# Optimization experiments

Hardware: AMD Instinct MI355X
Metric: run time of the kernel (lower is better)

Reference implementation:

```python
import jax, jax.numpy as jnp
import numpy as np

NUM_HEADS = 4
BN_EPS = 1e-5


def setup_inputs() -> dict:
    key = jax.random.key(0)
    k1, k2, k3 = jax.random.split(key, 3)
    B, C, H, W = 4, 512, 64, 64
    c_attn = 256
    x = jax.random.normal(k1, (B, C, H, W), dtype=jnp.float32)
    # 1x1 convs are plain channel matmuls: weight[out, in]
    w_qkv = jax.random.normal(k2, (3 * c_attn, c_attn), dtype=jnp.float32) * (c_attn ** -0.5)
    w_proj = jax.random.normal(k3, (c_attn, c_attn), dtype=jnp.float32) * (c_attn ** -0.5)
    gamma = jnp.ones((c_attn,), dtype=jnp.float32)
    beta = jnp.zeros((c_attn,), dtype=jnp.float32)
    return {"x": x, "w_qkv": w_qkv, "w_proj": w_proj, "gamma": gamma, "beta": beta}


def reference(x, w_qkv, w_proj, gamma, beta):
    B, C, H, W = x.shape
    c_attn = w_proj.shape[0]
    head_dim = c_attn // NUM_HEADS
    scale = head_dim ** -0.5
    N = H * W

    x_attn = x[:, :c_attn].reshape(B, c_attn, N)   # [B, c_attn, N]
    x_skip = x[:, c_attn:]                          # [B, c_skip, H, W]

    # 1x1 conv qkv (no bias): [B, 3*c_attn, N]
    qkv = jnp.einsum('oc,bcn->bon', w_qkv, x_attn)
    qkv = qkv.reshape(B, 3, NUM_HEADS, head_dim, N)
    q, k, v = qkv[:, 0], qkv[:, 1], qkv[:, 2]       # each [B, h, d, N]

    # attn[b,h,i,j] = sum_d q[b,h,d,i] * k[b,h,d,j] * scale
    attn = jnp.einsum('bhdn,bhdm->bhnm', q, k) * scale
    attn = jax.nn.softmax(attn, axis=-1)

    # out[b,h,d,i] = sum_j attn[b,h,i,j] * v[b,h,d,j]
    out = jnp.einsum('bhnm,bhdm->bhdn', attn, v).reshape(B, c_attn, N)

    # 1x1 conv proj (no bias)
    out = jnp.einsum('oc,bcn->bon', w_proj, out)

    # BatchNorm2d (training mode: batch statistics over B and spatial dims)
    mean = out.mean(axis=(0, 2), keepdims=True)
    var = out.var(axis=(0, 2), keepdims=True)  # biased variance, as torch BN
    out = (out - mean) * jax.lax.rsqrt(var + BN_EPS)
    out = out * gamma[None, :, None] + beta[None, :, None]

    out = out.reshape(B, c_attn, H, W)
    return jnp.concatenate([out, x_skip], axis=1)
```

## Files before the change

### kernel.cpp

```cpp
#include <hip/hip_runtime.h>
#include <stdint.h>

typedef float          f32x4  __attribute__((ext_vector_type(4)));
typedef __bf16         bf16x8 __attribute__((ext_vector_type(8)));
typedef unsigned short u16x4  __attribute__((ext_vector_type(4)));
typedef unsigned short u16x8  __attribute__((ext_vector_type(8)));

__device__ __forceinline__ float bf2f(unsigned short u) {
    union { uint32_t i; float f; } v; v.i = ((uint32_t)u) << 16; return v.f;
}
__device__ __forceinline__ unsigned short bfc(float f) {
    return __builtin_bit_cast(unsigned short, (__bf16)f);
}
__device__ __forceinline__ f32x4 mfma16(bf16x8 a, bf16x8 b, f32x4 c) {
    return __builtin_amdgcn_mfma_f32_16x16x32_bf16(a, b, c, 0, 0, 0);
}
__device__ __forceinline__ void async16(const unsigned short* g, unsigned short* l) {
    __builtin_amdgcn_global_load_lds(
        (const __attribute__((address_space(1))) void*)g,
        (__attribute__((address_space(3))) void*)l, 16, 0, 0);
}

#define QSC 0.18033688f

__global__ __launch_bounds__(256) void qkv_gemm(
    const float* __restrict__ x, const float* __restrict__ wqkv,
    unsigned short* __restrict__ Qb, unsigned short* __restrict__ Kb,
    unsigned short* __restrict__ Vb) {
    const int flat = (blockIdx.z * 32 + blockIdx.y) * 6 + blockIdx.x;
    const int v = (flat & 7) * 96 + (flat >> 3);
    const int mt = v % 6;
    const int rest = v / 6;
    const int nt = rest & 31;
    const int b  = rest >> 5;
    const int o0 = mt * 128, n0 = nt * 128;
    __shared__ __align__(16) unsigned short Wt[128 * 72];
    __shared__ __align__(16) unsigned short Xt[128 * 72];
    const int t = threadIdx.x;
    const int lane = t & 63, w = t >> 6;
    const int wr = w >> 1, wc = w & 1;
    const int l15 = lane & 15, g = lane >> 4;

    f32x4 acc[4][4];
    const f32x4 zero = {0.f, 0.f, 0.f, 0.f};
    for (int i = 0; i < 4; i++) for (int j = 0; j < 4; j++) acc[i][j] = zero;

    for (int k0 = 0; k0 < 256; k0 += 64) {
        {
            const int row = t >> 3, col = (t & 7) * 8;
            #pragma unroll
            for (int r = 0; r < 4; r++) {
                const float* p = wqkv + (size_t)(o0 + row + r * 32) * 256 + k0 + col;
                f32x4 v0 = *(const f32x4*)p;
                f32x4 v1 = *(const f32x4*)(p + 4);
                u16x8 o8 = { bfc(v0[0]), bfc(v0[1]), bfc(v0[2]), bfc(v0[3]),
                             bfc(v1[0]), bfc(v1[1]), bfc(v1[2]), bfc(v1[3]) };
                *(u16x8*)(&Wt[(row + r * 32) * 72 + col]) = o8;
            }
        }
        {
            const int cl = t >> 4, nl = (t & 15) * 8;
            const int xw = (t & 7) << 3;
            #pragma unroll
            for (int r = 0; r < 4; r++) {
                const int c = k0 + cl + r * 16;
                const int colw = (cl + r * 16) ^ xw;
                const float* p = x + (size_t)(b * 512 + c) * 4096 + n0 + nl;
                f32x4 v0 = *(const f32x4*)p;
                f32x4 v1 = *(const f32x4*)(p + 4);
                #pragma unroll
                for (int j = 0; j < 4; j++) Xt[(nl + j) * 72 + colw] = bfc(v0[j]);
                #pragma unroll
                for (int j = 0; j < 4; j++) Xt[(nl + 4 + j) * 72 + colw] = bfc(v1[j]);
            }
        }
        __syncthreads();
        #pragma unroll
        for (int kk = 0; kk < 2; kk++) {
            bf16x8 af[4], bfr[4];
            #pragma unroll
            for (int i = 0; i < 4; i++)
                af[i] = *(const bf16x8*)(&Wt[(wr * 64 + i * 16 + l15) * 72 + kk * 32 + g * 8]);
            #pragma unroll
            for (int j = 0; j < 4; j++) {
                const int rrow = wc * 64 + j * 16 + l15;
                const int xr = (((rrow >> 3) & 7) << 3);
                bfr[j] = *(const bf16x8*)(&Xt[rrow * 72 + ((kk * 32 + g * 8) ^ xr)]);
            }
            #pragma unroll
            for (int i = 0; i < 4; i++)
                #pragma unroll
                for (int j = 0; j < 4; j++)
                    acc[i][j] = mfma16(af[i], bfr[j], acc[i][j]);
        }
        __syncthreads();
    }

    #pragma unroll
    for (int i = 0; i < 4; i++) {
        const int o = o0 + wr * 64 + i * 16 + g * 4;
        #pragma unroll
        for (int j = 0; j < 4; j++) {
            const int n = n0 + wc * 64 + j * 16 + l15;
            f32x4 a = acc[i][j];
            if (o < 256) {
                u16x4 pv = { bfc(a[0] * QSC), bfc(a[1] * QSC), bfc(a[2] * QSC), bfc(a[3] * QSC) };
                const int h = o >> 6, d = o & 63;
                *(u16x4*)(&Qb[(((size_t)(b * 4 + h)) * 4096 + n) * 64 + d]) = pv;
            } else if (o < 512) {
                u16x4 pv = { bfc(a[0]), bfc(a[1]), bfc(a[2]), bfc(a[3]) };
                const int oo = o - 256; const int h = oo >> 6, d = oo & 63;
                *(u16x4*)(&Kb[(((size_t)(b * 4 + h)) * 4096 + n) * 64 + d]) = pv;
            } else {
                const int oo = o - 512; const int h = oo >> 6, d = oo & 63;
                const size_t base = (((size_t)(b * 4 + h)) * 64 + d) * 4096 + n;
                Vb[base] = bfc(a[0]); Vb[base + 4096] = bfc(a[1]);
                Vb[base + 8192] = bfc(a[2]); Vb[base + 12288] = bfc(a[3]);
            }
        }
    }
}

__global__ __launch_bounds__(256, 2) void flash_attn(
    const unsigned short* __restrict__ Qb, const unsigned short* __restrict__ Kb,
    const unsigned short* __restrict__ Vb, unsigned short* __restrict__ Opart,
    float* __restrict__ ml) {
    __shared__ __align__(16) unsigned short Kt[2][64 * 64];
    __shared__ __align__(16) unsigned short Vt[2][64 * 64];

    const int flat = (blockIdx.z * 16 + blockIdx.y) * 16 + blockIdx.x;
    const int nf = (flat & 7) * 64 + (flat >> 3);
    const int z  = nf >> 8;
    const int bh = (nf >> 4) & 15;
    const int nb = nf & 15;

    const int t = threadIdx.x, lane = t & 63, w = t >> 6;
    const int l15 = lane & 15, g = lane >> 4;
    const int xo = (l15 & 7) << 3;
    const int c0 = (g * 8) ^ xo, c1 = c0 ^ 32;
    const int vq = ((((g >> 1) ^ (l15 & 7)) << 3) | ((g & 1) << 2));

    const int rb = lane >> 3;
    const int cbe = ((lane & 7) ^ rb) << 3;
    const unsigned short* kgp = Kb + ((size_t)bh * 4096 + z * 2048 + w * 8 + rb) * 64 + cbe;
    const unsigned short* vgp = Vb + ((size_t)(bh * 64 + w * 8 + rb)) * 4096 + z * 2048 + cbe;

    auto stage = [&](int buf) {
        async16(kgp,          &Kt[buf][w * 512]);
        async16(kgp + 2048,   &Kt[buf][w * 512 + 2048]);
        async16(vgp,          &Vt[buf][w * 512]);
        async16(vgp + 131072, &Vt[buf][w * 512 + 2048]);
        kgp += 4096; vgp += 64;
    };

    bf16x8 qf[4][2];
    #pragma unroll
    for (int ntl = 0; ntl < 4; ++ntl) {
        const int nq = nb * 256 + w * 64 + ntl * 16 + l15;
        const unsigned short* qp = Qb + ((size_t)bh * 4096 + nq) * 64;
        qf[ntl][0] = *(const bf16x8*)(qp + g * 8);
        qf[ntl][1] = *(const bf16x8*)(qp + 32 + g * 8);
    }

    const bf16x8 ones8 = __builtin_bit_cast(bf16x8,
        (u16x8){0x3F80, 0x3F80, 0x3F80, 0x3F80, 0x3F80, 0x3F80, 0x3F80, 0x3F80});

    f32x4 of[4][4];
    f32x4 lf[4];
    const f32x4 zero = {0.f, 0.f, 0.f, 0.f};
    #pragma unroll
    for (int dt = 0; dt < 4; ++dt)
        #pragma unroll
        for (int ntl = 0; ntl < 4; ++ntl) of[dt][ntl] = zero;
    lf[0] = zero; lf[1] = zero; lf[2] = zero; lf[3] = zero;

    stage(0);
    __syncthreads();

    for (int itp = 0; itp < 16; ++itp) {
        #pragma unroll
        for (int cur = 0; cur < 2; ++cur) {
            if (itp * 2 + cur < 31) stage(cur ^ 1);

            bf16x8 ka[4][2], va[4][2];
            #pragma unroll
            for (int mt = 0; mt < 4; ++mt) {
                const int kro = (mt * 16 + l15) * 64;
                ka[mt][0] = *(const bf16x8*)(&Kt[cur][kro + c0]);
                ka[mt][1] = *(const bf16x8*)(&Kt[cur][kro + c1]);
            }
            #pragma unroll
            for (int dt = 0; dt < 4; ++dt) {
                const unsigned short* vr = &Vt[cur][l15 * 64 + dt * 1024];
                u16x4 w00 = *(const u16x4*)(vr + (vq ^ 0));
                u16x4 w01 = *(const u16x4*)(vr + (vq ^ 16));
                u16x4 w10 = *(const u16x4*)(vr + (vq ^ 32));
                u16x4 w11 = *(const u16x4*)(vr + (vq ^ 48));
                va[dt][0] = __builtin_bit_cast(bf16x8,
                    __builtin_shufflevector(w00, w01, 0, 1, 2, 3, 4, 5, 6, 7));
                va[dt][1] = __builtin_bit_cast(bf16x8,
                    __builtin_shufflevector(w10, w11, 0, 1, 2, 3, 4, 5, 6, 7));
            }

            #pragma unroll
            for (int ntl = 0; ntl < 4; ++ntl) {
                f32x4 st[4];
                __builtin_amdgcn_s_setprio(1);
                #pragma unroll
                for (int mt = 0; mt < 4; ++mt)
                    st[mt] = mfma16(ka[mt][1], qf[ntl][1],
                                    mfma16(ka[mt][0], qf[ntl][0], zero));
                __builtin_amdgcn_s_setprio(0);

                u16x4 q0 = { bfc(__builtin_amdgcn_exp2f(st[0][0])),
                             bfc(__builtin_amdgcn_exp2f(st[0][1])),
                             bfc(__builtin_amdgcn_exp2f(st[0][2])),
                             bfc(__builtin_amdgcn_exp2f(st[0][3])) };
                u16x4 q1 = { bfc(__builtin_amdgcn_exp2f(st[1][0])),
                             bfc(__builtin_amdgcn_exp2f(st[1][1])),
                             bfc(__builtin_amdgcn_exp2f(st[1][2])),
                             bfc(__builtin_amdgcn_exp2f(st[1][3])) };
                u16x4 q2 = { bfc(__builtin_amdgcn_exp2f(st[2][0])),
                             bfc(__builtin_amdgcn_exp2f(st[2][1])),
                             bfc(__builtin_amdgcn_exp2f(st[2][2])),
                             bfc(__builtin_amdgcn_exp2f(st[2][3])) };
                u16x4 q3 = { bfc(__builtin_amdgcn_exp2f(st[3][0])),
                             bfc(__builtin_amdgcn_exp2f(st[3][1])),
                             bfc(__builtin_amdgcn_exp2f(st[3][2])),
                             bfc(__builtin_amdgcn_exp2f(st[3][3])) };
                bf16x8 pb0 = __builtin_bit_cast(bf16x8,
                    __builtin_shufflevector(q0, q1, 0, 1, 2, 3, 4, 5, 6, 7));
                bf16x8 pb1 = __builtin_bit_cast(bf16x8,
                    __builtin_shufflevector(q2, q3, 0, 1, 2, 3, 4, 5, 6, 7));

                __builtin_amdgcn_s_setprio(1);
                lf[ntl] = mfma16(ones8, pb1, mfma16(ones8, pb0, lf[ntl]));
                #pragma unroll
                for (int dt = 0; dt < 4; ++dt)
                    of[dt][ntl] = mfma16(va[dt][1], pb1,
                                         mfma16(va[dt][0], pb0, of[dt][ntl]));
                __builtin_amdgcn_s_setprio(0);
            }
            __syncthreads();
        }
    }

    #pragma unroll
    for (int ntl = 0; ntl < 4; ++ntl) {
        const int nq = nb * 256 + w * 64 + ntl * 16 + l15;
        const size_t obase = ((size_t)((z * 16 + bh) * 4096 + nq)) * 64;
        #pragma unroll
        for (int dt = 0; dt < 4; ++dt) {
            u16x4 pv = { bfc(of[dt][ntl][0]), bfc(of[dt][ntl][1]),
                         bfc(of[dt][ntl][2]), bfc(of[dt][ntl][3]) };
            *(u16x4*)(&Opart[obase + dt * 16 + g * 4]) = pv;
        }
        if (g == 0) ml[z * 65536 + bh * 4096 + nq] = lf[ntl][0];
    }
}

__global__ __launch_bounds__(256) void proj_gemm(
    const unsigned short* __restrict__ Opart, const float* __restrict__ ml,
    const float* __restrict__ wproj,
    unsigned short* __restrict__ projbf, float* __restrict__ psum) {
    const int flat = (blockIdx.z * 32 + blockIdx.y) * 2 + blockIdx.x;
    const int v = (flat & 7) * 32 + (flat >> 3);
    const int mt = v & 1;
    const int rest = v >> 1;
    const int nt = rest & 31;
    const int b  = rest >> 5;
    const int o0 = mt * 128, n0 = nt * 128;
    __shared__ __align__(16) unsigned short Wt[128 * 72];
    __shared__ __align__(16) unsigned short Bt[128 * 72];
    const int t = threadIdx.x;
    const int lane = t & 63, w = t >> 6;
    const int wr = w >> 1, wc = w & 1;
    const int l15 = lane & 15, g = lane >> 4;

    f32x4 acc[4][4];
    const f32x4 zero = {0.f, 0.f, 0.f, 0.f};
    for (int i = 0; i < 4; i++) for (int j = 0; j < 4; j++) acc[i][j] = zero;

    for (int k0 = 0; k0 < 256; k0 += 64) {
        const int row = t >> 3, col = (t & 7) * 8;
        const int h = k0 >> 6;
        #pragma unroll
        for (int r = 0; r < 4; r++) {
            const float* p = wproj + (size_t)(o0 + row + r * 32) * 256 + k0 + col;
            f32x4 v0 = *(const f32x4*)p;
            f32x4 v1 = *(const f32x4*)(p + 4);
            u16x8 o8 = { bfc(v0[0]), bfc(v0[1]), bfc(v0[2]), bfc(v0[3]),
                         bfc(v1[0]), bfc(v1[1]), bfc(v1[2]), bfc(v1[3]) };
            *(u16x8*)(&Wt[(row + r * 32) * 72 + col]) = o8;
            const int n = n0 + row + r * 32;
            const int qidx = (b * 4 + h) * 4096 + n;
            const float inv = 1.f / (ml[qidx] + ml[65536 + qidx]);
            u16x8 m1 = *(const u16x8*)(Opart + (size_t)qidx * 64 + col);
            u16x8 m2 = *(const u16x8*)(Opart + 4194304u + (size_t)qidx * 64 + col);
            u16x8 a;
            #pragma unroll
            for (int j = 0; j < 8; ++j) a[j] = bfc((bf2f(m1[j]) + bf2f(m2[j])) * inv);
            *(u16x8*)(&Bt[(row + r * 32) * 72 + col]) = a;
        }
        __syncthreads();
        #pragma unroll
        for (int kk = 0; kk < 2; kk++) {
            bf16x8 af[4], bfr[4];
            #pragma unroll
            for (int i = 0; i < 4; i++)
                af[i] = *(const bf16x8*)(&Wt[(wr * 64 + i * 16 + l15) * 72 + kk * 32 + g * 8]);
            #pragma unroll
            for (int j = 0; j < 4; j++)
                bfr[j] = *(const bf16x8*)(&Bt[(wc * 64 + j * 16 + l15) * 72 + kk * 32 + g * 8]);
            #pragma unroll
            for (int i = 0; i < 4; i++)
                #pragma unroll
                for (int j = 0; j < 4; j++)
                    acc[i][j] = mfma16(af[i], bfr[j], acc[i][j]);
        }
        __syncthreads();
    }

    #pragma unroll
    for (int i = 0; i < 4; i++) {
        const int o = o0 + wr * 64 + i * 16 + g * 4;
        #pragma unroll
        for (int j = 0; j < 4; j++) {
            const int n = n0 + wc * 64 + j * 16 + l15;
            f32x4 a = acc[i][j];
            #pragma unroll
            for (int r = 0; r < 4; r++)
                projbf[((size_t)(b * 256 + o + r)) * 4096 + n] = bfc(a[r]);
        }
        f32x4 s = acc[i][0], q;
        #pragma unroll
        for (int r = 0; r < 4; ++r) q[r] = acc[i][0][r] * acc[i][0][r];
        #pragma unroll
        for (int j = 1; j < 4; ++j)
            #pragma unroll
            for (int r = 0; r < 4; ++r) {
                s[r] += acc[i][j][r];
                q[r] = fmaf(acc[i][j][r], acc[i][j][r], q[r]);
            }
        #pragma unroll
        for (int m = 1; m < 16; m <<= 1) {
            #pragma unroll
            for (int r = 0; r < 4; ++r) {
                s[r] += __shfl_xor(s[r], m, 64);
                q[r] += __shfl_xor(q[r], m, 64);
            }
        }
        if (l15 == 0) {
            const int slot = (b * 32 + nt) * 2 + wc;
            *(f32x4*)(&psum[slot * 256 + o]) = s;
            *(f32x4*)(&psum[65536 + slot * 256 + o]) = q;
        }
    }
}

__global__ __launch_bounds__(256) void bn_finalize(const float* __restrict__ psum,
                                                   float* __restrict__ stats) {
    const int o = blockIdx.x, t = threadIdx.x;
    const int lane = t & 63, w = t >> 6;
    float s = psum[t * 256 + o];
    float q = psum[65536 + t * 256 + o];
    #pragma unroll
    for (int m = 1; m < 64; m <<= 1) {
        s += __shfl_xor(s, m, 64);
        q += __shfl_xor(q, m, 64);
    }
    __shared__ float red[8];
    if (lane == 0) { red[w] = s; red[4 + w] = q; }
    __syncthreads();
    if (t == 0) {
        const float S = red[0] + red[1] + red[2] + red[3];
        const float Q = red[4] + red[5] + red[6] + red[7];
        const float mean = S * (1.f / 16384.f);
        const float var = Q * (1.f / 16384.f) - mean * mean;
        stats[o] = mean;
        stats[256 + o] = rsqrtf(var + 1e-5f);
    }
}

__global__ __launch_bounds__(256) void bn_apply(
    const unsigned short* __restrict__ projbf, const float* __restrict__ stats,
    const float* __restrict__ gamma, const float* __restrict__ beta,
    const float* __restrict__ x, float* __restrict__ out) {
    const size_t idx8 = ((size_t)blockIdx.x * 256 + threadIdx.x) * 8;
    const int n  = (int)(idx8 & 4095);
    const int ch = (int)((idx8 >> 12) & 511);
    const int b  = (int)(idx8 >> 21);
    if (ch < 256) {
        const float mean = stats[ch], rstd = stats[256 + ch];
        const float sc = gamma[ch] * rstd;
        const float sh = beta[ch] - mean * sc;
        u16x8 pv = *(const u16x8*)(projbf + (((size_t)(b * 256 + ch)) << 12) + n);
        f32x4 o0, o1;
        #pragma unroll
        for (int j = 0; j < 4; j++) { o0[j] = bf2f(pv[j]) * sc + sh; o1[j] = bf2f(pv[4 + j]) * sc + sh; }
        *(f32x4*)(out + idx8) = o0;
        *(f32x4*)(out + idx8 + 4) = o1;
    } else {
        *(f32x4*)(out + idx8)     = *(const f32x4*)(x + idx8);
        *(f32x4*)(out + idx8 + 4) = *(const f32x4*)(x + idx8 + 4);
    }
}

extern "C" void kernel_launch(void* const* d_in, const int* in_sizes, int n_in,
                              void* d_out, int out_size, void* d_ws, size_t ws_size,
                              hipStream_t stream) {
    const float* x     = (const float*)d_in[0];
    const float* wqkv  = (const float*)d_in[1];
    const float* wproj = (const float*)d_in[2];
    const float* gamma = (const float*)d_in[3];
    const float* beta  = (const float*)d_in[4];
    float* out = (float*)d_out;

    char* ws = (char*)d_ws;
    unsigned short* Qb     = (unsigned short*)(ws);
    unsigned short* Kb     = (unsigned short*)(ws + (8ull  << 20));
    unsigned short* Vb     = (unsigned short*)(ws + (16ull << 20));
    unsigned short* Opart  = (unsigned short*)(ws + (24ull << 20));
    float*          ml     = (float*)(ws + (41ull << 20));
    unsigned short* projbf = (unsigned short*)(ws);
    float*          psum   = (float*)(ws + (9ull << 20));
    float*          stats  = (float*)(ws + (9ull << 20) + (768u << 10));

    qkv_gemm   <<<dim3(6, 32, 4),  256, 0, stream>>>(x, wqkv, Qb, Kb, Vb);
    flash_attn <<<dim3(16, 16, 2), 256, 0, stream>>>(Qb, Kb, Vb, Opart, ml);
    proj_gemm  <<<dim3(2, 32, 4),  256, 0, stream>>>(Opart, ml, wproj, projbf, psum);
    bn_finalize<<<256,             256, 0, stream>>>(psum, stats);
    bn_apply   <<<4096,            256, 0, stream>>>(projbf, stats, gamma, beta, x, out);
}
```

Baseline: 118.5 us.

## Halve proj GEMM N-tile and fold BN finalize into bn_apply

The projection GEMM now uses 64-wide spatial tiles, which doubles the grid to 512 blocks to raise occupancy and parallelism, and doubles the number of partial-sum slots. The separate bn_finalize kernel is removed. Each bn_apply block for an attention channel now reduces the 512 partial sums itself before normalizing. This saves one kernel launch, but every attention-channel block repeats the statistics reduction, adding redundant psum reads and a block sync.

```diff
diff --git a/kernel.cpp b/kernel.cpp
--- a/kernel.cpp
+++ b/kernel.cpp
@@ -263,23 +263,23 @@
     const unsigned short* __restrict__ Opart, const float* __restrict__ ml,
     const float* __restrict__ wproj,
     unsigned short* __restrict__ projbf, float* __restrict__ psum) {
-    const int flat = (blockIdx.z * 32 + blockIdx.y) * 2 + blockIdx.x;
-    const int v = (flat & 7) * 32 + (flat >> 3);
+    const int flat = (blockIdx.z * 64 + blockIdx.y) * 2 + blockIdx.x;
+    const int v = (flat & 7) * 64 + (flat >> 3);
     const int mt = v & 1;
     const int rest = v >> 1;
-    const int nt = rest & 31;
-    const int b  = rest >> 5;
-    const int o0 = mt * 128, n0 = nt * 128;
+    const int nt = rest & 63;
+    const int b  = rest >> 6;
+    const int o0 = mt * 128, n0 = nt * 64;
     __shared__ __align__(16) unsigned short Wt[128 * 72];
-    __shared__ __align__(16) unsigned short Bt[128 * 72];
+    __shared__ __align__(16) unsigned short Bt[64 * 72];
     const int t = threadIdx.x;
     const int lane = t & 63, w = t >> 6;
     const int wr = w >> 1, wc = w & 1;
     const int l15 = lane & 15, g = lane >> 4;
 
-    f32x4 acc[4][4];
+    f32x4 acc[4][2];
     const f32x4 zero = {0.f, 0.f, 0.f, 0.f};
-    for (int i = 0; i < 4; i++) for (int j = 0; j < 4; j++) acc[i][j] = zero;
+    for (int i = 0; i < 4; i++) { acc[i][0] = zero; acc[i][1] = zero; }
 
     for (int k0 = 0; k0 < 256; k0 += 64) {
         const int row = t >> 3, col = (t & 7) * 8;
@@ -292,6 +292,9 @@
             u16x8 o8 = { bfc(v0[0]), bfc(v0[1]), bfc(v0[2]), bfc(v0[3]),
                          bfc(v1[0]), bfc(v1[1]), bfc(v1[2]), bfc(v1[3]) };
             *(u16x8*)(&Wt[(row + r * 32) * 72 + col]) = o8;
+        }
+        #pragma unroll
+        for (int r = 0; r < 2; r++) {
             const int n = n0 + row + r * 32;
             const int qidx = (b * 4 + h) * 4096 + n;
             const float inv = 1.f / (ml[qidx] + ml[65536 + qidx]);
@@ -305,17 +308,17 @@
         __syncthreads();
         #pragma unroll
         for (int kk = 0; kk < 2; kk++) {
-            bf16x8 af[4], bfr[4];
+            bf16x8 af[4], bfr[2];
             #pragma unroll
             for (int i = 0; i < 4; i++)
                 af[i] = *(const bf16x8*)(&Wt[(wr * 64 + i * 16 + l15) * 72 + kk * 32 + g * 8]);
             #pragma unroll
-            for (int j = 0; j < 4; j++)
-                bfr[j] = *(const bf16x8*)(&Bt[(wc * 64 + j * 16 + l15) * 72 + kk * 32 + g * 8]);
+            for (int j = 0; j < 2; j++)
+                bfr[j] = *(const bf16x8*)(&Bt[(wc * 32 + j * 16 + l15) * 72 + kk * 32 + g * 8]);
             #pragma unroll
             for (int i = 0; i < 4; i++)
                 #pragma unroll
-                for (int j = 0; j < 4; j++)
+                for (int j = 0; j < 2; j++)
                     acc[i][j] = mfma16(af[i], bfr[j], acc[i][j]);
         }
         __syncthreads();
@@ -325,8 +328,8 @@
     for (int i = 0; i < 4; i++) {
         const int o = o0 + wr * 64 + i * 16 + g * 4;
         #pragma unroll
-        for (int j = 0; j < 4; j++) {
-            const int n = n0 + wc * 64 + j * 16 + l15;
+        for (int j = 0; j < 2; j++) {
+            const int n = n0 + wc * 32 + j * 16 + l15;
             f32x4 a = acc[i][j];
             #pragma unroll
             for (int r = 0; r < 4; r++)
@@ -336,12 +339,10 @@
         #pragma unroll
         for (int r = 0; r < 4; ++r) q[r] = acc[i][0][r] * acc[i][0][r];
         #pragma unroll
-        for (int j = 1; j < 4; ++j)
-            #pragma unroll
-            for (int r = 0; r < 4; ++r) {
-                s[r] += acc[i][j][r];
-                q[r] = fmaf(acc[i][j][r], acc[i][j][r], q[r]);
-            }
+        for (int r = 0; r < 4; ++r) {
+            s[r] += acc[i][1][r];
+            q[r] = fmaf(acc[i][1][r], acc[i][1][r], q[r]);
+        }
         #pragma unroll
         for (int m = 1; m < 16; m <<= 1) {
             #pragma unroll
@@ -351,47 +352,39 @@
             }
         }
         if (l15 == 0) {
-            const int slot = (b * 32 + nt) * 2 + wc;
+            const int slot = (b * 64 + nt) * 2 + wc;
             *(f32x4*)(&psum[slot * 256 + o]) = s;
-            *(f32x4*)(&psum[65536 + slot * 256 + o]) = q;
-        }
-    }
-}
-
-__global__ __launch_bounds__(256) void bn_finalize(const float* __restrict__ psum,
-                                                   float* __restrict__ stats) {
-    const int o = blockIdx.x, t = threadIdx.x;
-    const int lane = t & 63, w = t >> 6;
-    float s = psum[t * 256 + o];
-    float q = psum[65536 + t * 256 + o];
-    #pragma unroll
-    for (int m = 1; m < 64; m <<= 1) {
-        s += __shfl_xor(s, m, 64);
-        q += __shfl_xor(q, m, 64);
-    }
-    __shared__ float red[8];
-    if (lane == 0) { red[w] = s; red[4 + w] = q; }
-    __syncthreads();
-    if (t == 0) {
-        const float S = red[0] + red[1] + red[2] + red[3];
-        const float Q = red[4] + red[5] + red[6] + red[7];
-        const float mean = S * (1.f / 16384.f);
-        const float var = Q * (1.f / 16384.f) - mean * mean;
-        stats[o] = mean;
-        stats[256 + o] = rsqrtf(var + 1e-5f);
+            *(f32x4*)(&psum[131072 + slot * 256 + o]) = q;
+        }
     }
 }
 
 __global__ __launch_bounds__(256) void bn_apply(
-    const unsigned short* __restrict__ projbf, const float* __restrict__ stats,
+    const unsigned short* __restrict__ projbf, const float* __restrict__ psum,
     const float* __restrict__ gamma, const float* __restrict__ beta,
     const float* __restrict__ x, float* __restrict__ out) {
-    const size_t idx8 = ((size_t)blockIdx.x * 256 + threadIdx.x) * 8;
+    const int t = threadIdx.x;
+    const size_t idx8 = ((size_t)blockIdx.x * 256 + t) * 8;
     const int n  = (int)(idx8 & 4095);
     const int ch = (int)((idx8 >> 12) & 511);
     const int b  = (int)(idx8 >> 21);
     if (ch < 256) {
-        const float mean = stats[ch], rstd = stats[256 + ch];
+        const int lane = t & 63, w = t >> 6;
+        float s = psum[t * 256 + ch] + psum[(t + 256) * 256 + ch];
+        float q = psum[131072 + t * 256 + ch] + psum[131072 + (t + 256) * 256 + ch];
+        #pragma unroll
+        for (int m = 1; m < 64; m <<= 1) {
+            s += __shfl_xor(s, m, 64);
+            q += __shfl_xor(q, m, 64);
+        }
+        __shared__ float red[8];
+        if (lane == 0) { red[w] = s; red[4 + w] = q; }
+        __syncthreads();
+        const float S = red[0] + red[1] + red[2] + red[3];
+        const float Q = red[4] + red[5] + red[6] + red[7];
+        const float mean = S * (1.f / 16384.f);
+        const float var  = Q * (1.f / 16384.f) - mean * mean;
+        const float rstd = rsqrtf(var + 1e-5f);
         const float sc = gamma[ch] * rstd;
         const float sh = beta[ch] - mean * sc;
         u16x8 pv = *(const u16x8*)(projbf + (((size_t)(b * 256 + ch)) << 12) + n);
@@ -424,11 +417,9 @@
     float*          ml     = (float*)(ws + (41ull << 20));
     unsigned short* projbf = (unsigned short*)(ws);
     float*          psum   = (float*)(ws + (9ull << 20));
-    float*          stats  = (float*)(ws + (9ull << 20) + (768u << 10));
-
-    qkv_gemm   <<<dim3(6, 32, 4),  256, 0, stream>>>(x, wqkv, Qb, Kb, Vb);
-    flash_attn <<<dim3(16, 16, 2), 256, 0, stream>>>(Qb, Kb, Vb, Opart, ml);
-    proj_gemm  <<<dim3(2, 32, 4),  256, 0, stream>>>(Opart, ml, wproj, projbf, psum);
-    bn_finalize<<<256,             256, 0, stream>>>(psum, stats);
-    bn_apply   <<<4096,            256, 0, stream>>>(projbf, stats, gamma, beta, x, out);
-}
+
+    qkv_gemm  <<<dim3(6, 32, 4),  256, 0, stream>>>(x, wqkv, Qb, Kb, Vb);
+    flash_attn<<<dim3(16, 16, 2), 256, 0, stream>>>(Qb, Kb, Vb, Opart, ml);
+    proj_gemm <<<dim3(2, 64, 4),  256, 0, stream>>>(Opart, ml, wproj, projbf, psum);
+    bn_apply  <<<4096,            256, 0, stream>>>(projbf, psum, gamma, beta, x, out);
+}
```

Measured after the change: 120.2 us. About the same (+1.4%).
